# Kernel optimization log

Measured on AMD Instinct MI355X. Metric: run time of the kernel, lower is better.

Reference implementation:

```python
import jax, jax.numpy as jnp
import numpy as np

N_NODES = 50000
N_EDGES = 1600000
N_OBS = 128
HIDDEN = 128
N_ACT = 32
K_OUT = 64


def gcn_conv(x, W, b, src, dst, n_nodes):
    """PyG GCNConv: out = D^{-1/2} (A + I) D^{-1/2} (x W) + b.

    Self-loop handled analytically (norm = 1/deg for the loop edge)
    instead of concatenating loop edges.
    """
    h = x @ W  # [N, out]
    # degree with self loops: in-degree + 1
    deg = jnp.zeros((n_nodes,), x.dtype).at[dst].add(jnp.ones((), x.dtype)) + 1.0
    dinv = jax.lax.rsqrt(deg)  # deg >= 1, safe
    norm = dinv[src] * dinv[dst]  # [E]
    agg = jax.ops.segment_sum(h[src] * norm[:, None], dst, num_segments=n_nodes)
    agg = agg + h * (dinv * dinv)[:, None]  # self-loop term: h / deg
    return agg + b


def setup_inputs() -> dict:
    key = jax.random.key(0)
    ks = jax.random.split(key, 6)
    x = jax.random.normal(ks[0], (N_OBS, N_NODES), dtype=jnp.float32)
    edge_index = jax.random.randint(ks[1], (2, N_EDGES), 0, N_NODES, dtype=jnp.int64)
    onehot_values = jax.random.uniform(ks[2], (K_OUT, N_NODES), dtype=jnp.float32)
    W1 = jax.random.normal(ks[3], (N_OBS, HIDDEN), dtype=jnp.float32) / np.sqrt(N_OBS)
    b1 = jnp.zeros((HIDDEN,), jnp.float32)
    W2 = jax.random.normal(ks[4], (HIDDEN, N_ACT), dtype=jnp.float32) / np.sqrt(HIDDEN)
    b2 = jnp.zeros((N_ACT,), jnp.float32)
    return {"x": x, "edge_index": edge_index, "onehot_values": onehot_values,
            "W1": W1, "b1": b1, "W2": W2, "b2": b2}


def reference(x, edge_index, onehot_values, W1, b1, W2, b2):
    # eval mode: dropout is identity
    src, dst = edge_index[0], edge_index[1]
    h = x.T  # graph.x.T -> [N, n_obs]
    h = jax.nn.relu(gcn_conv(h, W1, b1, src, dst, N_NODES))
    h = gcn_conv(h, W2, b2, src, dst, N_NODES)
    return onehot_values @ h  # [K_OUT, N_ACT]
```

## Files before the change

kernel.cpp:

```cpp
#include <hip/hip_runtime.h>

#define NN 50000
#define NE 1600000
#define NB 391
#define BSH 7
#define BCAP 4736

#define OFF_H1    0
#define OFF_AGG1  3200000
#define OFF_HW2   9600000
#define OFF_H2    10400000
#define OFF_DINV  12000000
#define OFF_ROWS  12050000
#define OFF_GCNT  12101000
#define OFF_GBASE 12101500
#define OFF_CSRC  12102000
#define OFF_BIN   13702000

typedef __attribute__((ext_vector_type(8))) short bf16x8;
typedef __attribute__((ext_vector_type(8))) unsigned short u16x8;
typedef __attribute__((ext_vector_type(4))) float f32x4;

__device__ __forceinline__ unsigned short f2b(float f) {
    unsigned u = __float_as_uint(f);
    u += 0x7fffu + ((u >> 16) & 1u);
    return (unsigned short)(u >> 16);
}
__device__ __forceinline__ float b2f(unsigned short h) {
    return __uint_as_float((unsigned)h << 16);
}
__device__ __forceinline__ float blo(unsigned u) { return __uint_as_float(u << 16); }
__device__ __forceinline__ float bhi(unsigned u) { return __uint_as_float(u & 0xffff0000u); }

__global__ __launch_bounds__(256) void k_binA(const int* __restrict__ ei,
                                              int* __restrict__ gcount,
                                              unsigned* __restrict__ binned) {
    __shared__ int hist[NB];
    const int t = threadIdx.x;
    for (int i = t; i < NB; i += 256) hist[i] = 0;
    __syncthreads();
    const int e0 = blockIdx.x * (NE / 256);
    const int e1 = e0 + (NE / 256);
    for (int e = e0 + t; e < e1; e += 256)
        atomicAdd(&hist[ei[NE + e] >> BSH], 1);
    __syncthreads();
    for (int i = t; i < NB; i += 256) {
        const int v = hist[i];
        hist[i] = atomicAdd(&gcount[i], v);
    }
    __syncthreads();
    for (int e = e0 + t; e < e1; e += 256) {
        const int s = ei[e], d = ei[NE + e];
        const int b = d >> BSH;
        const int pos = atomicAdd(&hist[b], 1);
        binned[(size_t)b * BCAP + pos] = (unsigned)s | ((unsigned)(d & 127) << 16);
    }
}

__global__ __launch_bounds__(512) void k_base(const int* __restrict__ gcount,
                                              int* __restrict__ gbase) {
    __shared__ int s[512];
    const int t = threadIdx.x;
    const int v = (t < NB) ? gcount[t] : 0;
    s[t] = v;
    __syncthreads();
    #pragma unroll
    for (int off = 1; off < 512; off <<= 1) {
        const int x = (t >= off) ? s[t - off] : 0;
        __syncthreads();
        s[t] += x;
        __syncthreads();
    }
    if (t < NB) gbase[t] = s[t] - v;
    if (t == NB - 1) gbase[NB] = s[t];
}

__global__ __launch_bounds__(256) void k_binB(const int* __restrict__ gcount,
                                              const int* __restrict__ gbase,
                                              const unsigned* __restrict__ binned,
                                              int* __restrict__ rows,
                                              float* __restrict__ dinv,
                                              int* __restrict__ csrc) {
    __shared__ int deg[128];
    __shared__ int ofs[128];
    __shared__ int scn[128];
    const int b = blockIdx.x, t = threadIdx.x;
    const int n0 = b << BSH;
    const int nloc = (NN - n0 < 128) ? (NN - n0) : 128;
    const int cnt = gcount[b];
    const int obase = gbase[b];
    const unsigned* eb = binned + (size_t)b * BCAP;
    if (t < 128) deg[t] = 0;
    __syncthreads();
    for (int i = t; i < cnt; i += 256) atomicAdd(&deg[eb[i] >> 16], 1);
    __syncthreads();
    if (t < 128) scn[t] = deg[t];
    __syncthreads();
    #pragma unroll
    for (int o = 1; o < 128; o <<= 1) {
        const int x = (t >= o && t < 128) ? scn[t - o] : 0;
        __syncthreads();
        if (t < 128) scn[t] += x;
        __syncthreads();
    }
    if (t < 128) {
        const int ep = scn[t] - deg[t];
        ofs[t] = ep;
        if (t < nloc) {
            rows[n0 + t] = obase + ep;
            dinv[n0 + t] = rsqrtf((float)deg[t] + 1.0f);
        }
    }
    if (b == NB - 1 && t == 0) rows[NN] = NE;
    __syncthreads();
    for (int i = t; i < cnt; i += 256) {
        const unsigned r = eb[i];
        const int local = atomicAdd(&ofs[r >> 16], 1);
        csrc[obase + local] = (int)(r & 0xffffu);
    }
}

__global__ __launch_bounds__(256) void k_w1t(const float* __restrict__ W1,
                                             unsigned short* __restrict__ w1t) {
    const int id = blockIdx.x * 1024 + threadIdx.x;
    #pragma unroll
    for (int i = 0; i < 4; ++i) {
        const int e = id + 256 * i;
        const int k = e >> 7, c = e & 127;
        w1t[c * 128 + k] = f2b(W1[e]);
    }
}

__global__ __launch_bounds__(256) void k_gemm1(const float* __restrict__ x,
                                               const unsigned short* __restrict__ w1t,
                                               const float* __restrict__ dinv,
                                               unsigned short* __restrict__ h1s) {
    __shared__ unsigned short lxs[64 * 136];
    const int t = threadIdx.x;
    const int gn0 = blockIdx.x * 64;
    {
        const int col = t & 63, kr = t >> 6;
        const int gn = gn0 + col;
        #pragma unroll
        for (int i = 0; i < 4; ++i) {
            const int k0 = kr * 32 + i * 8;
            u16x8 v;
            #pragma unroll
            for (int j = 0; j < 8; ++j) {
                const float xv = (gn < NN) ? x[(size_t)(k0 + j) * NN + gn] : 0.f;
                v[j] = f2b(xv);
            }
            *(u16x8*)&lxs[col * 136 + k0] = v;
        }
    }
    __syncthreads();
    const int w = t >> 6, l = t & 63;
    const int lr = l & 15, lg = l >> 4;
    const unsigned short* pa = &lxs[(w * 16 + lr) * 136 + lg * 8];
    f32x4 acc[8];
    #pragma unroll
    for (int ct = 0; ct < 8; ++ct) acc[ct] = (f32x4){0.f, 0.f, 0.f, 0.f};
    #pragma unroll
    for (int ks = 0; ks < 4; ++ks) {
        const bf16x8 av = *(const bf16x8*)&pa[ks * 32];
        const unsigned short* pw = &w1t[lr * 128 + ks * 32 + lg * 8];
        const bf16x8 b0 = *(const bf16x8*)&pw[0 * 16 * 128];
        const bf16x8 b1 = *(const bf16x8*)&pw[1 * 16 * 128];
        const bf16x8 b2 = *(const bf16x8*)&pw[2 * 16 * 128];
        const bf16x8 b3 = *(const bf16x8*)&pw[3 * 16 * 128];
        const bf16x8 b4 = *(const bf16x8*)&pw[4 * 16 * 128];
        const bf16x8 b5 = *(const bf16x8*)&pw[5 * 16 * 128];
        const bf16x8 b6 = *(const bf16x8*)&pw[6 * 16 * 128];
        const bf16x8 b7 = *(const bf16x8*)&pw[7 * 16 * 128];
        acc[0] = __builtin_amdgcn_mfma_f32_16x16x32_bf16(av, b0, acc[0], 0, 0, 0);
        acc[1] = __builtin_amdgcn_mfma_f32_16x16x32_bf16(av, b1, acc[1], 0, 0, 0);
        acc[2] = __builtin_amdgcn_mfma_f32_16x16x32_bf16(av, b2, acc[2], 0, 0, 0);
        acc[3] = __builtin_amdgcn_mfma_f32_16x16x32_bf16(av, b3, acc[3], 0, 0, 0);
        acc[4] = __builtin_amdgcn_mfma_f32_16x16x32_bf16(av, b4, acc[4], 0, 0, 0);
        acc[5] = __builtin_amdgcn_mfma_f32_16x16x32_bf16(av, b5, acc[5], 0, 0, 0);
        acc[6] = __builtin_amdgcn_mfma_f32_16x16x32_bf16(av, b6, acc[6], 0, 0, 0);
        acc[7] = __builtin_amdgcn_mfma_f32_16x16x32_bf16(av, b7, acc[7], 0, 0, 0);
    }
    __syncthreads();
    const int nl0 = w * 16 + lg * 4;
    const float4 dv = *(const float4*)&dinv[gn0 + nl0];
    const float dva[4] = {dv.x, dv.y, dv.z, dv.w};
    #pragma unroll
    for (int ct = 0; ct < 8; ++ct) {
        const int c = ct * 16 + lr;
        #pragma unroll
        for (int r = 0; r < 4; ++r)
            lxs[(nl0 + r) * 136 + c] = f2b(acc[ct][r] * dva[r]);
    }
    __syncthreads();
    {
        const int row = t >> 2, cb = (t & 3) * 32;
        const int gn = gn0 + row;
        if (gn < NN) {
            #pragma unroll
            for (int i = 0; i < 4; ++i)
                *(u16x8*)&h1s[(size_t)gn * 128 + cb + i * 8] =
                    *(const u16x8*)&lxs[row * 136 + cb + i * 8];
        }
    }
}

__global__ __launch_bounds__(256) void k_gather1(const int* __restrict__ rows,
                                                 const int* __restrict__ csrc,
                                                 const float* __restrict__ dinv,
                                                 const unsigned short* __restrict__ h1s,
                                                 unsigned short* __restrict__ ag1b) {
    const int n = __builtin_amdgcn_readfirstlane((blockIdx.x * 256 + threadIdx.x) >> 6);
    const int lane = threadIdx.x & 63;
    if (n >= NN) return;
    const int beg = rows[n], end = rows[n + 1];
    float ax0 = 0.f, ay0 = 0.f, ax1 = 0.f, ay1 = 0.f;
    float ax2 = 0.f, ay2 = 0.f, ax3 = 0.f, ay3 = 0.f;
    int p = beg;
    for (; p + 16 <= end; p += 16) {
        const int s0 = csrc[p + 0], s1 = csrc[p + 1], s2 = csrc[p + 2], s3 = csrc[p + 3];
        const int s4 = csrc[p + 4], s5 = csrc[p + 5], s6 = csrc[p + 6], s7 = csrc[p + 7];
        const int s8 = csrc[p + 8], s9 = csrc[p + 9], sa = csrc[p + 10], sb = csrc[p + 11];
        const int sc = csrc[p + 12], sd = csrc[p + 13], se = csrc[p + 14], sf = csrc[p + 15];
        const unsigned u0 = *(const unsigned*)&h1s[(size_t)s0 * 128 + lane * 2];
        const unsigned u1 = *(const unsigned*)&h1s[(size_t)s1 * 128 + lane * 2];
        const unsigned u2 = *(const unsigned*)&h1s[(size_t)s2 * 128 + lane * 2];
        const unsigned u3 = *(const unsigned*)&h1s[(size_t)s3 * 128 + lane * 2];
        const unsigned u4 = *(const unsigned*)&h1s[(size_t)s4 * 128 + lane * 2];
        const unsigned u5 = *(const unsigned*)&h1s[(size_t)s5 * 128 + lane * 2];
        const unsigned u6 = *(const unsigned*)&h1s[(size_t)s6 * 128 + lane * 2];
        const unsigned u7 = *(const unsigned*)&h1s[(size_t)s7 * 128 + lane * 2];
        const unsigned u8 = *(const unsigned*)&h1s[(size_t)s8 * 128 + lane * 2];
        const unsigned u9 = *(const unsigned*)&h1s[(size_t)s9 * 128 + lane * 2];
        const unsigned ua = *(const unsigned*)&h1s[(size_t)sa * 128 + lane * 2];
        const unsigned ub = *(const unsigned*)&h1s[(size_t)sb * 128 + lane * 2];
        const unsigned uc = *(const unsigned*)&h1s[(size_t)sc * 128 + lane * 2];
        const unsigned ud = *(const unsigned*)&h1s[(size_t)sd * 128 + lane * 2];
        const unsigned ue = *(const unsigned*)&h1s[(size_t)se * 128 + lane * 2];
        const unsigned uf = *(const unsigned*)&h1s[(size_t)sf * 128 + lane * 2];
        ax0 += blo(u0); ay0 += bhi(u0);
        ax1 += blo(u1); ay1 += bhi(u1);
        ax2 += blo(u2); ay2 += bhi(u2);
        ax3 += blo(u3); ay3 += bhi(u3);
        ax0 += blo(u4); ay0 += bhi(u4);
        ax1 += blo(u5); ay1 += bhi(u5);
        ax2 += blo(u6); ay2 += bhi(u6);
        ax3 += blo(u7); ay3 += bhi(u7);
        ax0 += blo(u8); ay0 += bhi(u8);
        ax1 += blo(u9); ay1 += bhi(u9);
        ax2 += blo(ua); ay2 += bhi(ua);
        ax3 += blo(ub); ay3 += bhi(ub);
        ax0 += blo(uc); ay0 += bhi(uc);
        ax1 += blo(ud); ay1 += bhi(ud);
        ax2 += blo(ue); ay2 += bhi(ue);
        ax3 += blo(uf); ay3 += bhi(uf);
    }
    for (; p + 4 <= end; p += 4) {
        const int s0 = csrc[p + 0], s1 = csrc[p + 1], s2 = csrc[p + 2], s3 = csrc[p + 3];
        const unsigned u0 = *(const unsigned*)&h1s[(size_t)s0 * 128 + lane * 2];
        const unsigned u1 = *(const unsigned*)&h1s[(size_t)s1 * 128 + lane * 2];
        const unsigned u2 = *(const unsigned*)&h1s[(size_t)s2 * 128 + lane * 2];
        const unsigned u3 = *(const unsigned*)&h1s[(size_t)s3 * 128 + lane * 2];
        ax0 += blo(u0); ay0 += bhi(u0);
        ax1 += blo(u1); ay1 += bhi(u1);
        ax2 += blo(u2); ay2 += bhi(u2);
        ax3 += blo(u3); ay3 += bhi(u3);
    }
    for (; p < end; ++p) {
        const int s = csrc[p];
        const unsigned u0 = *(const unsigned*)&h1s[(size_t)s * 128 + lane * 2];
        ax0 += blo(u0); ay0 += bhi(u0);
    }
    const float dn = dinv[n];
    const float sx = ((ax0 + ax1) + (ax2 + ax3)) * dn;
    const float sy = ((ay0 + ay1) + (ay2 + ay3)) * dn;
    const unsigned pk = (unsigned)f2b(sx) | ((unsigned)f2b(sy) << 16);
    *(unsigned*)&ag1b[(size_t)n * 128 + lane * 2] = pk;
}

__global__ __launch_bounds__(256) void k_fuse1(const unsigned short* __restrict__ ag1b,
                                               const unsigned short* __restrict__ h1s,
                                               const float* __restrict__ dinv,
                                               const float* __restrict__ b1,
                                               const float* __restrict__ W2,
                                               unsigned short* __restrict__ hw2s) {
    __shared__ float hs[32][132];
    __shared__ float w2s[128 * 32];
    const int t = threadIdx.x;
    const int n0 = blockIdx.x * 32;
    #pragma unroll
    for (int i = 0; i < 16; ++i) w2s[t + 256 * i] = W2[t + 256 * i];
    #pragma unroll
    for (int i = 0; i < 4; ++i) {
        const int idx4 = t + 256 * i;
        const int n = idx4 >> 5, c4 = (idx4 & 31) * 4;
        const int node = n0 + n;
        float4 r = make_float4(0.f, 0.f, 0.f, 0.f);
        if (node < NN) {
            const ushort4 au = *(const ushort4*)&ag1b[(size_t)node * 128 + c4];
            const ushort4 hu = *(const ushort4*)&h1s[(size_t)node * 128 + c4];
            const float dn = dinv[node];
            const float4 bb = *(const float4*)&b1[c4];
            r.x = fmaxf(fmaf(b2f(hu.x), dn, b2f(au.x)) + bb.x, 0.f);
            r.y = fmaxf(fmaf(b2f(hu.y), dn, b2f(au.y)) + bb.y, 0.f);
            r.z = fmaxf(fmaf(b2f(hu.z), dn, b2f(au.z)) + bb.z, 0.f);
            r.w = fmaxf(fmaf(b2f(hu.w), dn, b2f(au.w)) + bb.w, 0.f);
        }
        *(float4*)&hs[n][c4] = r;
    }
    __syncthreads();
    const int n = t >> 3, j4 = (t & 7) * 4;
    const int node = n0 + n;
    float acc[4] = {0.f, 0.f, 0.f, 0.f};
    #pragma unroll 8
    for (int k = 0; k < 128; ++k) {
        const float hv = hs[n][k];
        const float4 wv = *(const float4*)&w2s[k * 32 + j4];
        acc[0] = fmaf(hv, wv.x, acc[0]);
        acc[1] = fmaf(hv, wv.y, acc[1]);
        acc[2] = fmaf(hv, wv.z, acc[2]);
        acc[3] = fmaf(hv, wv.w, acc[3]);
    }
    if (node < NN) {
        const float ds = dinv[node];
        ushort4 pk;
        pk.x = f2b(acc[0] * ds); pk.y = f2b(acc[1] * ds);
        pk.z = f2b(acc[2] * ds); pk.w = f2b(acc[3] * ds);
        *(ushort4*)&hw2s[(size_t)node * 32 + j4] = pk;
    }
}

__global__ __launch_bounds__(256) void k_gather2(const int* __restrict__ rows,
                                                 const int* __restrict__ csrc,
                                                 const float* __restrict__ dinv,
                                                 const unsigned short* __restrict__ hw2s,
                                                 const float* __restrict__ b2,
                                                 float* __restrict__ h2) {
    const int n = __builtin_amdgcn_readfirstlane((blockIdx.x * 256 + threadIdx.x) >> 6);
    const int lane = threadIdx.x & 63;
    const int g = lane >> 4;
    const int c2 = (lane & 15) * 2;
    if (n >= NN) return;
    const int beg = rows[n], end = rows[n + 1];
    float ax0 = 0.f, ay0 = 0.f, ax1 = 0.f, ay1 = 0.f;
    float ax2 = 0.f, ay2 = 0.f, ax3 = 0.f, ay3 = 0.f;
    int p = beg;
    for (; p + 16 <= end; p += 16) {
        const int e0 = csrc[p + g + 0];
        const int e1 = csrc[p + g + 4];
        const int e2 = csrc[p + g + 8];
        const int e3 = csrc[p + g + 12];
        const unsigned u0 = *(const unsigned*)&hw2s[(size_t)e0 * 32 + c2];
        const unsigned u1 = *(const unsigned*)&hw2s[(size_t)e1 * 32 + c2];
        const unsigned u2 = *(const unsigned*)&hw2s[(size_t)e2 * 32 + c2];
        const unsigned u3 = *(const unsigned*)&hw2s[(size_t)e3 * 32 + c2];
        ax0 += blo(u0); ay0 += bhi(u0);
        ax1 += blo(u1); ay1 += bhi(u1);
        ax2 += blo(u2); ay2 += bhi(u2);
        ax3 += blo(u3); ay3 += bhi(u3);
    }
    if (p + 8 <= end) {
        const int e0 = csrc[p + g + 0];
        const int e1 = csrc[p + g + 4];
        const unsigned u0 = *(const unsigned*)&hw2s[(size_t)e0 * 32 + c2];
        const unsigned u1 = *(const unsigned*)&hw2s[(size_t)e1 * 32 + c2];
        ax0 += blo(u0); ay0 += bhi(u0);
        ax1 += blo(u1); ay1 += bhi(u1);
        p += 8;
    }
    for (; p < end; p += 4) {
        if (g < end - p) {
            const int e = csrc[p + g];
            const unsigned u = *(const unsigned*)&hw2s[(size_t)e * 32 + c2];
            ax0 += blo(u); ay0 += bhi(u);
        }
    }
    float sx = (ax0 + ax1) + (ax2 + ax3);
    float sy = (ay0 + ay1) + (ay2 + ay3);
    sx += __shfl_xor(sx, 16); sx += __shfl_xor(sx, 32);
    sy += __shfl_xor(sy, 16); sy += __shfl_xor(sy, 32);
    if (lane < 16) {
        const float dn = dinv[n];
        const unsigned su = *(const unsigned*)&hw2s[(size_t)n * 32 + c2];
        const float2 bb = *(const float2*)&b2[c2];
        float2 r;
        r.x = fmaf(sx + blo(su), dn, bb.x);
        r.y = fmaf(sy + bhi(su), dn, bb.y);
        *(float2*)&h2[(size_t)n * 32 + c2] = r;
    }
}

__global__ __launch_bounds__(256) void k_final(const float* __restrict__ O,
                                               const float* __restrict__ h2,
                                               float* __restrict__ out) {
    __shared__ float h2s[128][32];
    __shared__ float Os[64][128];
    const int t = threadIdx.x;
    const int n0 = blockIdx.x * 128;
    #pragma unroll
    for (int i = 0; i < 16; ++i) {
        const int idx = t + 256 * i;
        const int n = idx >> 5, j = idx & 31;
        const int node = n0 + n;
        h2s[n][j] = (node < NN) ? h2[(size_t)node * 32 + j] : 0.f;
    }
    #pragma unroll
    for (int i = 0; i < 32; ++i) {
        const int idx = t + 256 * i;
        const int r = idx >> 7, c = idx & 127;
        const int node = n0 + c;
        Os[r][c] = (node < NN) ? O[(size_t)r * NN + node] : 0.f;
    }
    __syncthreads();
    const int j = t & 31, k0 = (t >> 5) * 8;
    float acc[8];
    #pragma unroll
    for (int i = 0; i < 8; ++i) acc[i] = 0.f;
    for (int n = 0; n < 128; ++n) {
        const float hv = h2s[n][j];
        #pragma unroll
        for (int i = 0; i < 8; ++i) acc[i] = fmaf(Os[k0 + i][n], hv, acc[i]);
    }
    #pragma unroll
    for (int i = 0; i < 8; ++i) atomicAdd(&out[(k0 + i) * 32 + j], acc[i]);
}

extern "C" void kernel_launch(void* const* d_in, const int* in_sizes, int n_in,
                              void* d_out, int out_size, void* d_ws, size_t ws_size,
                              hipStream_t stream) {
    const float* x  = (const float*)d_in[0];
    const int*   ei = (const int*)d_in[1];
    const float* O  = (const float*)d_in[2];
    const float* W1 = (const float*)d_in[3];
    const float* b1 = (const float*)d_in[4];
    const float* W2 = (const float*)d_in[5];
    const float* b2 = (const float*)d_in[6];
    float* out = (float*)d_out;

    float* wsf = (float*)d_ws;
    unsigned short* h1s  = (unsigned short*)(wsf + OFF_H1);
    unsigned short* ag1b = (unsigned short*)(wsf + OFF_AGG1);
    unsigned short* hw2s = (unsigned short*)(wsf + OFF_HW2);
    float*          h2   = wsf + OFF_H2;
    float* dinv  = wsf + OFF_DINV;
    int*   rows  = (int*)(wsf + OFF_ROWS);
    int*   gcnt  = (int*)(wsf + OFF_GCNT);
    int*   gbase = (int*)(wsf + OFF_GBASE);
    int*   csrc  = (int*)(wsf + OFF_CSRC);
    unsigned* binned = (unsigned*)(wsf + OFF_BIN);
    unsigned short* w1t = (unsigned short*)(wsf + OFF_BIN);

    hipMemsetAsync(gcnt, 0, NB * 4, stream);

    k_binA<<<256, 256, 0, stream>>>(ei, gcnt, binned);
    k_base<<<1, 512, 0, stream>>>(gcnt, gbase);
    k_binB<<<NB, 256, 0, stream>>>(gcnt, gbase, binned, rows, dinv, csrc);

    k_w1t<<<16, 256, 0, stream>>>(W1, w1t);
    k_gemm1<<<(NN + 63) / 64, 256, 0, stream>>>(x, w1t, dinv, h1s);
    k_gather1<<<(NN * 64 + 255) / 256, 256, 0, stream>>>(rows, csrc, dinv, h1s, ag1b);
    k_fuse1<<<(NN + 31) / 32, 256, 0, stream>>>(ag1b, h1s, dinv, b1, W2, hw2s);
    k_gather2<<<(NN * 64 + 255) / 256, 256, 0, stream>>>(rows, csrc, dinv, hw2s, b2, h2);

    hipMemsetAsync(out, 0, (size_t)out_size * 4, stream);
    k_final<<<(NN + 127) / 128, 256, 0, stream>>>(O, h2, out);
}
```

Baseline: 190.8 us.

## Fuse layer-1 gather with bias/ReLU and W2 projection into one kernel

Merges the layer-1 neighbor gather, self-loop/bias/ReLU epilogue and the 128x32 W2 matmul into a single kernel, removing the bf16 ag1b intermediate write and its re-read along with one launch. W2 is pre-converted to bf16 alongside W1 in a combined conversion kernel, and each block loads it into shared memory. Each block now handles only 4 nodes, so every block reloads the 8KB W2 tile, and only half the threads do the small per-node matmul, which adds redundant shared-memory traffic and idle lanes.

New measurement: 182.5 us. -4.4%, faster.

```diff
diff --git a/kernel.cpp b/kernel.cpp
--- a/kernel.cpp
+++ b/kernel.cpp
@@ -7,7 +7,6 @@
 #define BCAP 4736
 
 #define OFF_H1    0
-#define OFF_AGG1  3200000
 #define OFF_HW2   9600000
 #define OFF_H2    10400000
 #define OFF_DINV  12000000
@@ -120,14 +119,25 @@
     }
 }
 
-__global__ __launch_bounds__(256) void k_w1t(const float* __restrict__ W1,
-                                             unsigned short* __restrict__ w1t) {
-    const int id = blockIdx.x * 1024 + threadIdx.x;
-    #pragma unroll
-    for (int i = 0; i < 4; ++i) {
-        const int e = id + 256 * i;
-        const int k = e >> 7, c = e & 127;
-        w1t[c * 128 + k] = f2b(W1[e]);
+__global__ __launch_bounds__(256) void k_wconv(const float* __restrict__ W1,
+                                               const float* __restrict__ W2,
+                                               unsigned short* __restrict__ w1t,
+                                               unsigned short* __restrict__ w2t) {
+    const int t = threadIdx.x;
+    if (blockIdx.x < 16) {
+        const int id = blockIdx.x * 1024 + t;
+        #pragma unroll
+        for (int i = 0; i < 4; ++i) {
+            const int e = id + 256 * i;
+            const int k = e >> 7, c = e & 127;
+            w1t[c * 128 + k] = f2b(W1[e]);
+        }
+    } else {
+        #pragma unroll
+        for (int i = 0; i < 16; ++i) {
+            const int e = t + 256 * i;
+            w2t[e] = f2b(W2[e]);
+        }
     }
 }
 
@@ -205,128 +215,104 @@
     }
 }
 
-__global__ __launch_bounds__(256) void k_gather1(const int* __restrict__ rows,
-                                                 const int* __restrict__ csrc,
-                                                 const float* __restrict__ dinv,
-                                                 const unsigned short* __restrict__ h1s,
-                                                 unsigned short* __restrict__ ag1b) {
-    const int n = __builtin_amdgcn_readfirstlane((blockIdx.x * 256 + threadIdx.x) >> 6);
-    const int lane = threadIdx.x & 63;
-    if (n >= NN) return;
-    const int beg = rows[n], end = rows[n + 1];
-    float ax0 = 0.f, ay0 = 0.f, ax1 = 0.f, ay1 = 0.f;
-    float ax2 = 0.f, ay2 = 0.f, ax3 = 0.f, ay3 = 0.f;
-    int p = beg;
-    for (; p + 16 <= end; p += 16) {
-        const int s0 = csrc[p + 0], s1 = csrc[p + 1], s2 = csrc[p + 2], s3 = csrc[p + 3];
-        const int s4 = csrc[p + 4], s5 = csrc[p + 5], s6 = csrc[p + 6], s7 = csrc[p + 7];
-        const int s8 = csrc[p + 8], s9 = csrc[p + 9], sa = csrc[p + 10], sb = csrc[p + 11];
-        const int sc = csrc[p + 12], sd = csrc[p + 13], se = csrc[p + 14], sf = csrc[p + 15];
-        const unsigned u0 = *(const unsigned*)&h1s[(size_t)s0 * 128 + lane * 2];
-        const unsigned u1 = *(const unsigned*)&h1s[(size_t)s1 * 128 + lane * 2];
-        const unsigned u2 = *(const unsigned*)&h1s[(size_t)s2 * 128 + lane * 2];
-        const unsigned u3 = *(const unsigned*)&h1s[(size_t)s3 * 128 + lane * 2];
-        const unsigned u4 = *(const unsigned*)&h1s[(size_t)s4 * 128 + lane * 2];
-        const unsigned u5 = *(const unsigned*)&h1s[(size_t)s5 * 128 + lane * 2];
-        const unsigned u6 = *(const unsigned*)&h1s[(size_t)s6 * 128 + lane * 2];
-        const unsigned u7 = *(const unsigned*)&h1s[(size_t)s7 * 128 + lane * 2];
-        const unsigned u8 = *(const unsigned*)&h1s[(size_t)s8 * 128 + lane * 2];
-        const unsigned u9 = *(const unsigned*)&h1s[(size_t)s9 * 128 + lane * 2];
-        const unsigned ua = *(const unsigned*)&h1s[(size_t)sa * 128 + lane * 2];
-        const unsigned ub = *(const unsigned*)&h1s[(size_t)sb * 128 + lane * 2];
-        const unsigned uc = *(const unsigned*)&h1s[(size_t)sc * 128 + lane * 2];
-        const unsigned ud = *(const unsigned*)&h1s[(size_t)sd * 128 + lane * 2];
-        const unsigned ue = *(const unsigned*)&h1s[(size_t)se * 128 + lane * 2];
-        const unsigned uf = *(const unsigned*)&h1s[(size_t)sf * 128 + lane * 2];
-        ax0 += blo(u0); ay0 += bhi(u0);
-        ax1 += blo(u1); ay1 += bhi(u1);
-        ax2 += blo(u2); ay2 += bhi(u2);
-        ax3 += blo(u3); ay3 += bhi(u3);
-        ax0 += blo(u4); ay0 += bhi(u4);
-        ax1 += blo(u5); ay1 += bhi(u5);
-        ax2 += blo(u6); ay2 += bhi(u6);
-        ax3 += blo(u7); ay3 += bhi(u7);
-        ax0 += blo(u8); ay0 += bhi(u8);
-        ax1 += blo(u9); ay1 += bhi(u9);
-        ax2 += blo(ua); ay2 += bhi(ua);
-        ax3 += blo(ub); ay3 += bhi(ub);
-        ax0 += blo(uc); ay0 += bhi(uc);
-        ax1 += blo(ud); ay1 += bhi(ud);
-        ax2 += blo(ue); ay2 += bhi(ue);
-        ax3 += blo(uf); ay3 += bhi(uf);
-    }
-    for (; p + 4 <= end; p += 4) {
-        const int s0 = csrc[p + 0], s1 = csrc[p + 1], s2 = csrc[p + 2], s3 = csrc[p + 3];
-        const unsigned u0 = *(const unsigned*)&h1s[(size_t)s0 * 128 + lane * 2];
-        const unsigned u1 = *(const unsigned*)&h1s[(size_t)s1 * 128 + lane * 2];
-        const unsigned u2 = *(const unsigned*)&h1s[(size_t)s2 * 128 + lane * 2];
-        const unsigned u3 = *(const unsigned*)&h1s[(size_t)s3 * 128 + lane * 2];
-        ax0 += blo(u0); ay0 += bhi(u0);
-        ax1 += blo(u1); ay1 += bhi(u1);
-        ax2 += blo(u2); ay2 += bhi(u2);
-        ax3 += blo(u3); ay3 += bhi(u3);
-    }
-    for (; p < end; ++p) {
-        const int s = csrc[p];
-        const unsigned u0 = *(const unsigned*)&h1s[(size_t)s * 128 + lane * 2];
-        ax0 += blo(u0); ay0 += bhi(u0);
-    }
-    const float dn = dinv[n];
-    const float sx = ((ax0 + ax1) + (ax2 + ax3)) * dn;
-    const float sy = ((ay0 + ay1) + (ay2 + ay3)) * dn;
-    const unsigned pk = (unsigned)f2b(sx) | ((unsigned)f2b(sy) << 16);
-    *(unsigned*)&ag1b[(size_t)n * 128 + lane * 2] = pk;
-}
-
-__global__ __launch_bounds__(256) void k_fuse1(const unsigned short* __restrict__ ag1b,
-                                               const unsigned short* __restrict__ h1s,
-                                               const float* __restrict__ dinv,
-                                               const float* __restrict__ b1,
-                                               const float* __restrict__ W2,
-                                               unsigned short* __restrict__ hw2s) {
-    __shared__ float hs[32][132];
-    __shared__ float w2s[128 * 32];
-    const int t = threadIdx.x;
-    const int n0 = blockIdx.x * 32;
-    #pragma unroll
-    for (int i = 0; i < 16; ++i) w2s[t + 256 * i] = W2[t + 256 * i];
-    #pragma unroll
-    for (int i = 0; i < 4; ++i) {
-        const int idx4 = t + 256 * i;
-        const int n = idx4 >> 5, c4 = (idx4 & 31) * 4;
-        const int node = n0 + n;
-        float4 r = make_float4(0.f, 0.f, 0.f, 0.f);
+__global__ __launch_bounds__(256) void k_gf1(const int* __restrict__ rows,
+                                             const int* __restrict__ csrc,
+                                             const float* __restrict__ dinv,
+                                             const unsigned short* __restrict__ h1s,
+                                             const float* __restrict__ b1,
+                                             const unsigned short* __restrict__ w2t,
+                                             unsigned short* __restrict__ hw2s) {
+    __shared__ unsigned short w2l[128 * 32];
+    __shared__ unsigned short h1l[4][128];
+    const int t = threadIdx.x;
+    ((u16x8*)w2l)[t]       = ((const u16x8*)w2t)[t];
+    ((u16x8*)w2l)[t + 256] = ((const u16x8*)w2t)[t + 256];
+    const int wid = t >> 6, lane = t & 63;
+    const int n = __builtin_amdgcn_readfirstlane(blockIdx.x * 4 + wid);
+    float vx = 0.f, vy = 0.f;
+    if (n < NN) {
+        const int beg = rows[n], end = rows[n + 1];
+        float ax0 = 0.f, ay0 = 0.f, ax1 = 0.f, ay1 = 0.f;
+        float ax2 = 0.f, ay2 = 0.f, ax3 = 0.f, ay3 = 0.f;
+        int p = beg;
+        for (; p + 16 <= end; p += 16) {
+            const int s0 = csrc[p + 0], s1 = csrc[p + 1], s2 = csrc[p + 2], s3 = csrc[p + 3];
+            const int s4 = csrc[p + 4], s5 = csrc[p + 5], s6 = csrc[p + 6], s7 = csrc[p + 7];
+            const int s8 = csrc[p + 8], s9 = csrc[p + 9], sa = csrc[p + 10], sb = csrc[p + 11];
+            const int sc = csrc[p + 12], sd = csrc[p + 13], se = csrc[p + 14], sf = csrc[p + 15];
+            const unsigned u0 = *(const unsigned*)&h1s[(size_t)s0 * 128 + lane * 2];
+            const unsigned u1 = *(const unsigned*)&h1s[(size_t)s1 * 128 + lane * 2];
+            const unsigned u2 = *(const unsigned*)&h1s[(size_t)s2 * 128 + lane * 2];
+            const unsigned u3 = *(const unsigned*)&h1s[(size_t)s3 * 128 + lane * 2];
+            const unsigned u4 = *(const unsigned*)&h1s[(size_t)s4 * 128 + lane * 2];
+            const unsigned u5 = *(const unsigned*)&h1s[(size_t)s5 * 128 + lane * 2];
+            const unsigned u6 = *(const unsigned*)&h1s[(size_t)s6 * 128 + lane * 2];
+            const unsigned u7 = *(const unsigned*)&h1s[(size_t)s7 * 128 + lane * 2];
+            const unsigned u8 = *(const unsigned*)&h1s[(size_t)s8 * 128 + lane * 2];
+            const unsigned u9 = *(const unsigned*)&h1s[(size_t)s9 * 128 + lane * 2];
+            const unsigned ua = *(const unsigned*)&h1s[(size_t)sa * 128 + lane * 2];
+            const unsigned ub = *(const unsigned*)&h1s[(size_t)sb * 128 + lane * 2];
+            const unsigned uc = *(const unsigned*)&h1s[(size_t)sc * 128 + lane * 2];
+            const unsigned ud = *(const unsigned*)&h1s[(size_t)sd * 128 + lane * 2];
+            const unsigned ue = *(const unsigned*)&h1s[(size_t)se * 128 + lane * 2];
+            const unsigned uf = *(const unsigned*)&h1s[(size_t)sf * 128 + lane * 2];
+            ax0 += blo(u0); ay0 += bhi(u0);
+            ax1 += blo(u1); ay1 += bhi(u1);
+            ax2 += blo(u2); ay2 += bhi(u2);
+            ax3 += blo(u3); ay3 += bhi(u3);
+            ax0 += blo(u4); ay0 += bhi(u4);
+            ax1 += blo(u5); ay1 += bhi(u5);
+            ax2 += blo(u6); ay2 += bhi(u6);
+            ax3 += blo(u7); ay3 += bhi(u7);
+            ax0 += blo(u8); ay0 += bhi(u8);
+            ax1 += blo(u9); ay1 += bhi(u9);
+            ax2 += blo(ua); ay2 += bhi(ua);
+            ax3 += blo(ub); ay3 += bhi(ub);
+            ax0 += blo(uc); ay0 += bhi(uc);
+            ax1 += blo(ud); ay1 += bhi(ud);
+            ax2 += blo(ue); ay2 += bhi(ue);
+            ax3 += blo(uf); ay3 += bhi(uf);
+        }
+        for (; p + 4 <= end; p += 4) {
+            const int s0 = csrc[p + 0], s1 = csrc[p + 1], s2 = csrc[p + 2], s3 = csrc[p + 3];
+            const unsigned u0 = *(const unsigned*)&h1s[(size_t)s0 * 128 + lane * 2];
+            const unsigned u1 = *(const unsigned*)&h1s[(size_t)s1 * 128 + lane * 2];
+            const unsigned u2 = *(const unsigned*)&h1s[(size_t)s2 * 128 + lane * 2];
+            const unsigned u3 = *(const unsigned*)&h1s[(size_t)s3 * 128 + lane * 2];
+            ax0 += blo(u0); ay0 += bhi(u0);
+            ax1 += blo(u1); ay1 += bhi(u1);
+            ax2 += blo(u2); ay2 += bhi(u2);
+            ax3 += blo(u3); ay3 += bhi(u3);
+        }
+        for (; p < end; ++p) {
+            const int s = csrc[p];
+            const unsigned u0 = *(const unsigned*)&h1s[(size_t)s * 128 + lane * 2];
+            ax0 += blo(u0); ay0 += bhi(u0);
+        }
+        const float dn = dinv[n];
+        const float sx = ((ax0 + ax1) + (ax2 + ax3)) * dn;
+        const float sy = ((ay0 + ay1) + (ay2 + ay3)) * dn;
+        const unsigned su = *(const unsigned*)&h1s[(size_t)n * 128 + lane * 2];
+        const float2 bb = *(const float2*)&b1[lane * 2];
+        vx = fmaxf(fmaf(blo(su), dn, sx) + bb.x, 0.f);
+        vy = fmaxf(fmaf(bhi(su), dn, sy) + bb.y, 0.f);
+    }
+    *(unsigned*)&h1l[wid][lane * 2] = (unsigned)f2b(vx) | ((unsigned)f2b(vy) << 16);
+    __syncthreads();
+    if (t < 128) {
+        const int nd = t >> 5, j = t & 31;
+        const int node = blockIdx.x * 4 + nd;
         if (node < NN) {
-            const ushort4 au = *(const ushort4*)&ag1b[(size_t)node * 128 + c4];
-            const ushort4 hu = *(const ushort4*)&h1s[(size_t)node * 128 + c4];
-            const float dn = dinv[node];
-            const float4 bb = *(const float4*)&b1[c4];
-            r.x = fmaxf(fmaf(b2f(hu.x), dn, b2f(au.x)) + bb.x, 0.f);
-            r.y = fmaxf(fmaf(b2f(hu.y), dn, b2f(au.y)) + bb.y, 0.f);
-            r.z = fmaxf(fmaf(b2f(hu.z), dn, b2f(au.z)) + bb.z, 0.f);
-            r.w = fmaxf(fmaf(b2f(hu.w), dn, b2f(au.w)) + bb.w, 0.f);
-        }
-        *(float4*)&hs[n][c4] = r;
-    }
-    __syncthreads();
-    const int n = t >> 3, j4 = (t & 7) * 4;
-    const int node = n0 + n;
-    float acc[4] = {0.f, 0.f, 0.f, 0.f};
-    #pragma unroll 8
-    for (int k = 0; k < 128; ++k) {
-        const float hv = hs[n][k];
-        const float4 wv = *(const float4*)&w2s[k * 32 + j4];
-        acc[0] = fmaf(hv, wv.x, acc[0]);
-        acc[1] = fmaf(hv, wv.y, acc[1]);
-        acc[2] = fmaf(hv, wv.z, acc[2]);
-        acc[3] = fmaf(hv, wv.w, acc[3]);
-    }
-    if (node < NN) {
-        const float ds = dinv[node];
-        ushort4 pk;
-        pk.x = f2b(acc[0] * ds); pk.y = f2b(acc[1] * ds);
-        pk.z = f2b(acc[2] * ds); pk.w = f2b(acc[3] * ds);
-        *(ushort4*)&hw2s[(size_t)node * 32 + j4] = pk;
+            float acc = 0.f;
+            const unsigned* hp = (const unsigned*)&h1l[nd][0];
+            #pragma unroll 8
+            for (int k2 = 0; k2 < 64; ++k2) {
+                const unsigned hv = hp[k2];
+                acc = fmaf(blo(hv), b2f(w2l[(2 * k2) * 32 + j]), acc);
+                acc = fmaf(bhi(hv), b2f(w2l[(2 * k2 + 1) * 32 + j]), acc);
+            }
+            hw2s[(size_t)node * 32 + j] = f2b(acc * dinv[node]);
+        }
     }
 }
 
@@ -439,7 +425,6 @@
 
     float* wsf = (float*)d_ws;
     unsigned short* h1s  = (unsigned short*)(wsf + OFF_H1);
-    unsigned short* ag1b = (unsigned short*)(wsf + OFF_AGG1);
     unsigned short* hw2s = (unsigned short*)(wsf + OFF_HW2);
     float*          h2   = wsf + OFF_H2;
     float* dinv  = wsf + OFF_DINV;
@@ -449,6 +434,7 @@
     int*   csrc  = (int*)(wsf + OFF_CSRC);
     unsigned* binned = (unsigned*)(wsf + OFF_BIN);
     unsigned short* w1t = (unsigned short*)(wsf + OFF_BIN);
+    unsigned short* w2t = (unsigned short*)(wsf + OFF_BIN) + 16384;
 
     hipMemsetAsync(gcnt, 0, NB * 4, stream);
 
@@ -456,10 +442,9 @@
     k_base<<<1, 512, 0, stream>>>(gcnt, gbase);
     k_binB<<<NB, 256, 0, stream>>>(gcnt, gbase, binned, rows, dinv, csrc);
 
-    k_w1t<<<16, 256, 0, stream>>>(W1, w1t);
+    k_wconv<<<17, 256, 0, stream>>>(W1, W2, w1t, w2t);
     k_gemm1<<<(NN + 63) / 64, 256, 0, stream>>>(x, w1t, dinv, h1s);
-    k_gather1<<<(NN * 64 + 255) / 256, 256, 0, stream>>>(rows, csrc, dinv, h1s, ag1b);
-    k_fuse1<<<(NN + 31) / 32, 256, 0, stream>>>(ag1b, h1s, dinv, b1, W2, hw2s);
+    k_gf1<<<(NN + 3) / 4, 256, 0, stream>>>(rows, csrc, dinv, h1s, b1, w2t, hw2s);
     k_gather2<<<(NN * 64 + 255) / 256, 256, 0, stream>>>(rows, csrc, dinv, hw2s, b2, h2);
 
     hipMemsetAsync(out, 0, (size_t)out_size * 4, stream);
```
